# Optimization experiments

Measured on AMD Instinct MI355X. Metric: run time of the kernel, lower is better.

The kernel has to match this reference:

```python
import jax, jax.numpy as jnp
import numpy as np
import math

RATIOS = [2, 4, 8, 16]   # attn_aggr_ratio per path
HEAD_DIM = 64
EPS = 1e-5               # BatchNorm1d eps (eval mode, running stats)


def _bn(x, g, b, m, v):
    # x: (N, C, L); per-channel eval-mode BatchNorm1d
    inv = g / jnp.sqrt(v + EPS)
    return x * inv[None, :, None] + (b - m * inv)[None, :, None]


def _conv1(x, W, b=None):
    # 1x1 Conv1d == channel matmul. x: (N, Cin, L), W: (Cout, Cin)
    y = jnp.einsum('ncl,dc->ndl', x, W)
    if b is not None:
        y = y + b[None, :, None]
    return y


def setup_inputs() -> dict:
    key = jax.random.key(0)
    ks = iter(jax.random.split(key, 16))
    N, C, L = 8, 512, 3072
    P, d = 4, C // 4
    FF = 4 * C
    w = lambda shape: jax.random.normal(next(ks), shape, dtype=jnp.float32) * 0.05
    inp = {'x': jax.random.normal(next(ks), (N, C, L), dtype=jnp.float32)}
    for nm in ('norm1', 'norm2'):
        inp[nm + '_g'] = jnp.ones((C,), jnp.float32)
        inp[nm + '_b'] = jnp.zeros((C,), jnp.float32)
        inp[nm + '_m'] = jnp.zeros((C,), jnp.float32)
        inp[nm + '_v'] = jnp.ones((C,), jnp.float32)
    for nm in ('Wq', 'Wk', 'Wv', 'Wo', 'Wp'):
        inp[nm] = w((P, d, d))
    for nm in ('bq', 'bk', 'bv', 'bo'):
        inp[nm] = jnp.zeros((P, d), jnp.float32)
    for nm in ('ag', 'an'):  # aggr-block BN and pre-KV BN, per path
        inp[nm + '_g'] = jnp.ones((P, d), jnp.float32)
        inp[nm + '_b'] = jnp.zeros((P, d), jnp.float32)
        inp[nm + '_m'] = jnp.zeros((P, d), jnp.float32)
        inp[nm + '_v'] = jnp.ones((P, d), jnp.float32)
    inp['W1'] = w((FF, C)); inp['b1'] = jnp.zeros((FF,), jnp.float32)
    inp['W2'] = w((C, FF)); inp['b2'] = jnp.zeros((C,), jnp.float32)
    return inp


def reference(x, norm1_g, norm1_b, norm1_m, norm1_v,
              Wq, bq, Wk, bk, Wv, bv, Wo, bo, Wp,
              ag_g, ag_b, ag_m, ag_v, an_g, an_b, an_m, an_v,
              norm2_g, norm2_b, norm2_m, norm2_v,
              W1, b1, W2, b2):
    N, C, L = x.shape
    P = len(RATIOS)
    d = C // P
    h = _bn(x, norm1_g, norm1_b, norm1_m, norm1_v)
    outs = []
    for i, r in enumerate(RATIOS):  # small fixed set of paths
        xi = h[:, i * d:(i + 1) * d, :]                       # (N, d, L)
        q = _conv1(xi, Wq[i], bq[i])                          # (N, d, L)
        # local aware aggregation: avg_pool + max_pool (L divisible by r)
        xp = xi.reshape(N, d, L // r, r)
        xa = xp.mean(-1) + xp.max(-1)                         # (N, d, L/r)
        xa = _bn(_conv1(xa, Wp[i]), ag_g[i], ag_b[i], ag_m[i], ag_v[i])
        xa = _bn(xa, an_g[i], an_b[i], an_m[i], an_v[i])
        k = _conv1(xa, Wk[i], bk[i])
        v = _conv1(xa, Wv[i], bv[i])
        Nh = d // HEAD_DIM
        Lk = L // r
        qh = q.reshape(N, Nh, HEAD_DIM, L) / math.sqrt(HEAD_DIM)
        kh = k.reshape(N, Nh, HEAD_DIM, Lk)
        vh = v.reshape(N, Nh, HEAD_DIM, Lk)
        attn = jax.nn.softmax(jnp.einsum('nhel,nhem->nhlm', qh, kh), axis=-1)
        o = jnp.einsum('nhlm,nhem->nhel', attn, vh).reshape(N, d, L)
        outs.append(_conv1(o, Wo[i], bo[i]))
    x = x + jnp.concatenate(outs, axis=1)                     # residual
    h2 = _bn(x, norm2_g, norm2_b, norm2_m, norm2_v)
    m = jax.nn.gelu(_conv1(h2, W1, b1))
    m = _conv1(m, W2, b2)
    return x + m
```

## Files before the change

kernel.cpp:

```cpp
#include <hip/hip_runtime.h>
#include <math.h>

#define EPS 1e-5f

#define F_BIAS  1
#define F_DBN   2
#define F_GELU  4
#define F_RESID 8

typedef __attribute__((ext_vector_type(8))) __bf16 bf16x8;
typedef __attribute__((ext_vector_type(4))) float f32x4;
typedef __attribute__((ext_vector_type(8))) unsigned short u16x8;

__device__ __forceinline__ unsigned int pack2bf(float a, float b) {
    unsigned short ua = __builtin_bit_cast(unsigned short, (__bf16)a);
    unsigned short ub = __builtin_bit_cast(unsigned short, (__bf16)b);
    return (unsigned int)ua | ((unsigned int)ub << 16);
}

__device__ __forceinline__ void gload_lds16(const unsigned short* g, unsigned short* l) {
    __builtin_amdgcn_global_load_lds(
        (const __attribute__((address_space(1))) unsigned int*)g,
        (__attribute__((address_space(3))) unsigned int*)l,
        16, 0, 0);
}

__device__ __forceinline__ float gelu_f(float u) {
    float s = u * u;
    float w = u * fmaf(s, 0.0713548162726f, 1.59576912161f);
    float e = __expf(-w);
    return u * __builtin_amdgcn_rcpf(1.f + e);
}

__device__ __constant__ int c_LKS[4]  = {1536, 768, 384, 192};
__device__ __constant__ int c_OFFB[4] = {0, 1572864, 2359296, 2752512};

__global__ __launch_bounds__(256) void wcvt_kernel(
    const float* __restrict__ Wq, const float* __restrict__ Wk,
    const float* __restrict__ Wv, const float* __restrict__ Wo,
    const float* __restrict__ Wp, const float* __restrict__ W1,
    const float* __restrict__ W2, unsigned short* __restrict__ dst)
{
    const int WSZ = 65536;
    const int FSZ = 1048576;
    int i4 = blockIdx.x * blockDim.x + threadIdx.x;
    long long i = (long long)i4 * 4;
    const long long total = 5LL * WSZ + 2LL * FSZ;
    if (i >= total) return;
    #pragma unroll
    for (int j = 0; j < 4; ++j) {
        long long idx = i + j;
        float v;
        if      (idx < WSZ)            v = Wq[idx];
        else if (idx < 2 * WSZ)        v = Wk[idx - WSZ];
        else if (idx < 3 * WSZ)        v = Wv[idx - 2 * WSZ];
        else if (idx < 4 * WSZ)        v = Wo[idx - 3 * WSZ];
        else if (idx < 5 * WSZ)        v = Wp[idx - 4 * WSZ];
        else if (idx < 5 * WSZ + FSZ)  v = W1[idx - 5 * WSZ];
        else                           v = W2[idx - 5 * WSZ - FSZ];
        dst[idx] = __builtin_bit_cast(unsigned short, (__bf16)v);
    }
}

__global__ __launch_bounds__(256) void bn_transpose_kernel(
    const float* __restrict__ x,
    const float* __restrict__ g, const float* __restrict__ b,
    const float* __restrict__ bm, const float* __restrict__ bvv,
    unsigned short* __restrict__ hT, int C, int L)
{
    __shared__ float ps[64][65];
    const int l0 = blockIdx.x * 64, ct = blockIdx.y, n = blockIdx.z;
    const int tid = threadIdx.x;
    const int c = tid >> 2, q = tid & 3;
    const int cg = ct * 64 + c;
    float inv = g[cg] * rsqrtf(bvv[cg] + EPS);
    float add = b[cg] - bm[cg] * inv;
    const float* xp = x + ((size_t)n * C + cg) * L + l0 + q * 16;
    #pragma unroll
    for (int s = 0; s < 4; ++s) {
        float4 vv = *(const float4*)&xp[s * 4];
        ps[c][q * 16 + s * 4 + 0] = fmaf(vv.x, inv, add);
        ps[c][q * 16 + s * 4 + 1] = fmaf(vv.y, inv, add);
        ps[c][q * 16 + s * 4 + 2] = fmaf(vv.z, inv, add);
        ps[c][q * 16 + s * 4 + 3] = fmaf(vv.w, inv, add);
    }
    __syncthreads();
    #pragma unroll
    for (int j = 0; j < 2; ++j) {
        int row = (tid >> 3) + 32 * j;
        int cc0 = (tid & 7) * 8;
        unsigned int w0 = pack2bf(ps[cc0 + 0][row], ps[cc0 + 1][row]);
        unsigned int w1 = pack2bf(ps[cc0 + 2][row], ps[cc0 + 3][row]);
        unsigned int w2 = pack2bf(ps[cc0 + 4][row], ps[cc0 + 5][row]);
        unsigned int w3 = pack2bf(ps[cc0 + 6][row], ps[cc0 + 7][row]);
        *(uint4*)&hT[((size_t)n * L + l0 + row) * C + ct * 64 + cc0] =
            make_uint4(w0, w1, w2, w3);
    }
}

__global__ __launch_bounds__(256) void pool_bn_all_kernel(
    const float* __restrict__ x,
    const float* __restrict__ g, const float* __restrict__ b,
    const float* __restrict__ bm, const float* __restrict__ bvv,
    unsigned short* __restrict__ xa0T_all, int C, int L)
{
    const int p = blockIdx.z & 3;
    const int n = blockIdx.z >> 2;
    const int Lk = c_LKS[p];
    const int lk0 = blockIdx.x * 64;
    if (lk0 >= Lk) return;
    const int r = L / Lk;
    const int ct = blockIdx.y;
    __shared__ float ps[64][65];
    const int tid = threadIdx.x;
    const int c = tid >> 2, q = tid & 3;
    const int cg = p * 128 + ct * 64 + c;
    float inv = g[cg] * rsqrtf(bvv[cg] + EPS);
    float add = b[cg] - bm[cg] * inv;
    const float* xp = x + ((size_t)n * C + cg) * L;
    float rinv = 1.0f / (float)r;
    #pragma unroll
    for (int s = 0; s < 16; ++s) {
        int lk = q * 16 + s;
        const float* base = xp + (size_t)(lk0 + lk) * r;
        float sum = 0.f, mx = -INFINITY;
        for (int j = 0; j < r; j += 2) {
            float2 vv = *(const float2*)&base[j];
            float t0 = fmaf(vv.x, inv, add);
            float t1 = fmaf(vv.y, inv, add);
            sum += t0 + t1;
            mx = fmaxf(mx, fmaxf(t0, t1));
        }
        ps[c][lk] = sum * rinv + mx;
    }
    __syncthreads();
    unsigned short* dst = xa0T_all + c_OFFB[p];
    #pragma unroll
    for (int j = 0; j < 2; ++j) {
        int row = (tid >> 3) + 32 * j;
        int cc0 = (tid & 7) * 8;
        unsigned int w0 = pack2bf(ps[cc0 + 0][row], ps[cc0 + 1][row]);
        unsigned int w1 = pack2bf(ps[cc0 + 2][row], ps[cc0 + 3][row]);
        unsigned int w2 = pack2bf(ps[cc0 + 4][row], ps[cc0 + 5][row]);
        unsigned int w3 = pack2bf(ps[cc0 + 6][row], ps[cc0 + 7][row]);
        *(uint4*)&dst[((size_t)n * Lk + lk0 + row) * 128 + ct * 64 + cc0] =
            make_uint4(w0, w1, w2, w3);
    }
}

template<int OMODE>
__global__ __launch_bounds__(256) void gemm_bf(
    const unsigned short* __restrict__ A, const unsigned short* __restrict__ BT,
    int M, int K, int Npos, int ldBT, long long strideBT,
    const float* __restrict__ bias, float oscale, int flags,
    const float* __restrict__ g1, const float* __restrict__ b1p,
    const float* __restrict__ m1p, const float* __restrict__ v1p,
    const float* __restrict__ g2, const float* __restrict__ b2p,
    const float* __restrict__ m2p, const float* __restrict__ v2p,
    float* __restrict__ outN, long long strideN,
    const float* __restrict__ resid, long long strideR,
    unsigned short* __restrict__ outT, int ldT, int moff, long long strideT,
    int gKoff)
{
    __shared__ __align__(16) unsigned short As[2][128][32];
    __shared__ __align__(16) unsigned short Bs[2][128][32];

    const int tid = threadIdx.x;

    const int gdx = gridDim.x, gdy = gridDim.y;
    const int nwg = gdx * gdy * gridDim.z;
    int bid = blockIdx.x + gdx * (blockIdx.y + gdy * blockIdx.z);
    {
        int q = nwg >> 3, rr = nwg & 7;
        int xcd = bid & 7, idx = bid >> 3;
        bid = (xcd < rr ? xcd * (q + 1) : rr * (q + 1) + (xcd - rr) * q) + idx;
    }
    const int bx = bid % gdx;
    const int by = (bid / gdx) % gdy;
    const int bz = bid / (gdx * gdy);

    const int m0 = by * 128;
    const int p0 = bx * 128;
    const unsigned short* Bn = BT + (size_t)bz * strideBT
                              + (size_t)(m0 >> 7) * gKoff;

    const int wave = tid >> 6;
    const int lane = tid & 63;
    const int qcol = lane & 15;
    const int hi   = lane >> 4;
    const int wr   = wave >> 1;
    const int wc   = wave & 1;
    const int lrow = lane >> 2;
    const int lseg = (lane & 3) * 8;

    const unsigned short* aR0 = A + (size_t)(m0 + wave * 32 + lrow) * K + lseg;
    const unsigned short* aR1 = aR0 + (size_t)16 * K;
    int pr0 = p0 + wave * 32 + lrow;      if (pr0 > Npos - 1) pr0 = Npos - 1;
    int pr1 = p0 + wave * 32 + 16 + lrow; if (pr1 > Npos - 1) pr1 = Npos - 1;
    const unsigned short* bR0 = Bn + (size_t)pr0 * ldBT + lseg;
    const unsigned short* bR1 = Bn + (size_t)pr1 * ldBT + lseg;
    unsigned short* ldsA0 = &As[0][wave * 32][0];
    unsigned short* ldsA1 = &As[0][wave * 32 + 16][0];
    unsigned short* ldsB0 = &Bs[0][wave * 32][0];
    unsigned short* ldsB1 = &Bs[0][wave * 32 + 16][0];
    const int bufStride = 128 * 32;

    auto STAGE = [&](int b, int t) {
        const int ko = t * 32;
        gload_lds16(aR0 + ko, ldsA0 + b * bufStride);
        gload_lds16(aR1 + ko, ldsA1 + b * bufStride);
        gload_lds16(bR0 + ko, ldsB0 + b * bufStride);
        gload_lds16(bR1 + ko, ldsB1 + b * bufStride);
    };

    f32x4 acc[4][4] = {};
    const int nt = K >> 5;

    STAGE(0, 0);
    STAGE(1, 1);

    auto MFMA_STEP = [&](int b) {
        bf16x8 af[4], bfr[4];
        #pragma unroll
        for (int mi = 0; mi < 4; ++mi)
            af[mi] = *(const bf16x8*)&As[b][wr * 64 + mi * 16 + qcol][hi * 8];
        #pragma unroll
        for (int ni = 0; ni < 4; ++ni)
            bfr[ni] = *(const bf16x8*)&Bs[b][wc * 64 + ni * 16 + qcol][hi * 8];
        #pragma unroll
        for (int mi = 0; mi < 4; ++mi)
            #pragma unroll
            for (int ni = 0; ni < 4; ++ni)
                acc[mi][ni] = __builtin_amdgcn_mfma_f32_16x16x32_bf16(
                    af[mi], bfr[ni], acc[mi][ni], 0, 0, 0);
    };

    int cur = 0;
    for (int t = 0; t < nt - 1; ++t) {
        asm volatile("s_waitcnt vmcnt(4)" ::: "memory");
        __builtin_amdgcn_s_barrier();
        MFMA_STEP(cur);
        __builtin_amdgcn_s_barrier();
        if (t + 2 < nt) STAGE(cur, t + 2);
        cur ^= 1;
    }
    asm volatile("s_waitcnt vmcnt(0)" ::: "memory");
    __builtin_amdgcn_s_barrier();
    MFMA_STEP(cur);

    float* Cn = outN + (size_t)bz * strideN;
    const float* Rn = resid + (size_t)bz * strideR;
    unsigned short* Tn = outT + (size_t)bz * strideT;

    #pragma unroll
    for (int mi = 0; mi < 4; ++mi) {
        const int mb = m0 + wr * 64 + mi * 16 + hi * 4;
        float4 bv4 = make_float4(0.f, 0.f, 0.f, 0.f);
        if (flags & F_BIAS) bv4 = *(const float4*)&bias[mb];
        float s1[4], t1[4];
        if ((flags & F_DBN) || OMODE == 3) {
            float4 gg = *(const float4*)&g1[mb];
            float4 bb = *(const float4*)&b1p[mb];
            float4 mm = *(const float4*)&m1p[mb];
            float4 vv = *(const float4*)&v1p[mb];
            float gga[4] = {gg.x, gg.y, gg.z, gg.w};
            float bba[4] = {bb.x, bb.y, bb.z, bb.w};
            float mma[4] = {mm.x, mm.y, mm.z, mm.w};
            float vva[4] = {vv.x, vv.y, vv.z, vv.w};
            #pragma unroll
            for (int r2 = 0; r2 < 4; ++r2) {
                float iv = gga[r2] * rsqrtf(vva[r2] + EPS);
                s1[r2] = iv; t1[r2] = bba[r2] - mma[r2] * iv;
            }
        }
        float s2[4], t2[4];
        if (flags & F_DBN) {
            float4 gg = *(const float4*)&g2[mb];
            float4 bb = *(const float4*)&b2p[mb];
            float4 mm = *(const float4*)&m2p[mb];
            float4 vv = *(const float4*)&v2p[mb];
            float gga[4] = {gg.x, gg.y, gg.z, gg.w};
            float bba[4] = {bb.x, bb.y, bb.z, bb.w};
            float mma[4] = {mm.x, mm.y, mm.z, mm.w};
            float vva[4] = {vv.x, vv.y, vv.z, vv.w};
            #pragma unroll
            for (int r2 = 0; r2 < 4; ++r2) {
                float iv = gga[r2] * rsqrtf(vva[r2] + EPS);
                s2[r2] = iv; t2[r2] = bba[r2] - mma[r2] * iv;
            }
        }
        const float ba[4] = {bv4.x, bv4.y, bv4.z, bv4.w};
        #pragma unroll
        for (int ni = 0; ni < 4; ++ni) {
            const int cp = p0 + wc * 64 + ni * 16 + qcol;
            if (cp >= Npos) continue;
            float vals[4];
            #pragma unroll
            for (int r2 = 0; r2 < 4; ++r2) {
                float val = (acc[mi][ni][r2] + ba[r2]) * oscale;
                if (flags & F_DBN) {
                    val = fmaf(val, s1[r2], t1[r2]);
                    val = fmaf(val, s2[r2], t2[r2]);
                }
                if (flags & F_GELU) val = gelu_f(val);
                vals[r2] = val;
            }
            if (OMODE == 0 || OMODE == 3) {
                #pragma unroll
                for (int r2 = 0; r2 < 4; ++r2) {
                    size_t off = (size_t)(mb + r2) * Npos + cp;
                    float v = vals[r2];
                    if (flags & F_RESID) v += Rn[off];
                    Cn[off] = v;
                    vals[r2] = v;
                }
            }
            if (OMODE == 1) {
                *(uint2*)&Tn[(size_t)cp * ldT + moff + mb] =
                    make_uint2(pack2bf(vals[0], vals[1]), pack2bf(vals[2], vals[3]));
            }
            if (OMODE == 2) {
                #pragma unroll
                for (int r2 = 0; r2 < 4; ++r2)
                    Tn[(size_t)(mb + r2) * Npos + cp] =
                        __builtin_bit_cast(unsigned short, (__bf16)vals[r2]);
            }
            if (OMODE == 3) {
                float a0 = fmaf(vals[0], s1[0], t1[0]);
                float a1 = fmaf(vals[1], s1[1], t1[1]);
                float a2 = fmaf(vals[2], s1[2], t1[2]);
                float a3 = fmaf(vals[3], s1[3], t1[3]);
                *(uint2*)&Tn[(size_t)cp * ldT + moff + mb] =
                    make_uint2(pack2bf(a0, a1), pack2bf(a2, a3));
            }
        }
    }
}

template<int MODE>
__global__ __launch_bounds__(256) void gemm_path(
    const unsigned short* __restrict__ A0, const unsigned short* __restrict__ A1,
    const unsigned short* __restrict__ Bsrc,
    const float* __restrict__ bias0, const float* __restrict__ bias1,
    const float* __restrict__ agg, const float* __restrict__ agb,
    const float* __restrict__ agm, const float* __restrict__ agv,
    const float* __restrict__ ang, const float* __restrict__ anb,
    const float* __restrict__ anm, const float* __restrict__ anv,
    unsigned short* __restrict__ out0, unsigned short* __restrict__ out1)
{
    __shared__ __align__(16) unsigned short As[2][128][32];
    __shared__ __align__(16) unsigned short Bs[2][128][32];

    const int tid = threadIdx.x;
    const int gdx = gridDim.x, gdy = gridDim.y;
    const int nwg = gdx * gdy * gridDim.z;
    int bid = blockIdx.x + gdx * (blockIdx.y + gdy * blockIdx.z);
    {
        int q = nwg >> 3, rr = nwg & 7;
        int xcd = bid & 7, idx = bid >> 3;
        bid = (xcd < rr ? xcd * (q + 1) : rr * (q + 1) + (xcd - rr) * q) + idx;
    }
    const int bx = bid % gdx;
    const int by = (bid / gdx) % gdy;
    const int bz = bid / (gdx * gdy);

    int p, px;
    if      (bx < 12) { p = 0; px = bx; }
    else if (bx < 18) { p = 1; px = bx - 12; }
    else if (bx < 21) { p = 2; px = bx - 18; }
    else              { p = 3; px = bx - 21; }
    const int Lk = c_LKS[p];
    const int offb = c_OFFB[p];
    const int c0 = p * 128;
    const int p0 = px * 128;
    const int K = 128;

    const unsigned short* A = (MODE == 1 && by == 1 ? A1 : A0) + p * 16384;
    const unsigned short* Bn = Bsrc + offb + (size_t)bz * Lk * 128;

    const int wave = tid >> 6;
    const int lane = tid & 63;
    const int qcol = lane & 15;
    const int hi   = lane >> 4;
    const int wr   = wave >> 1;
    const int wc   = wave & 1;
    const int lrow = lane >> 2;
    const int lseg = (lane & 3) * 8;

    const unsigned short* aR0 = A + (size_t)(wave * 32 + lrow) * K + lseg;
    const unsigned short* aR1 = aR0 + (size_t)16 * K;
    int pr0 = p0 + wave * 32 + lrow;      if (pr0 > Lk - 1) pr0 = Lk - 1;
    int pr1 = p0 + wave * 32 + 16 + lrow; if (pr1 > Lk - 1) pr1 = Lk - 1;
    const unsigned short* bR0 = Bn + (size_t)pr0 * 128 + lseg;
    const unsigned short* bR1 = Bn + (size_t)pr1 * 128 + lseg;
    unsigned short* ldsA0 = &As[0][wave * 32][0];
    unsigned short* ldsA1 = &As[0][wave * 32 + 16][0];
    unsigned short* ldsB0 = &Bs[0][wave * 32][0];
    unsigned short* ldsB1 = &Bs[0][wave * 32 + 16][0];
    const int bufStride = 128 * 32;

    auto STAGE = [&](int b, int t) {
        const int ko = t * 32;
        gload_lds16(aR0 + ko, ldsA0 + b * bufStride);
        gload_lds16(aR1 + ko, ldsA1 + b * bufStride);
        gload_lds16(bR0 + ko, ldsB0 + b * bufStride);
        gload_lds16(bR1 + ko, ldsB1 + b * bufStride);
    };

    f32x4 acc[4][4] = {};
    STAGE(0, 0);
    STAGE(1, 1);

    auto MFMA_STEP = [&](int b) {
        bf16x8 af[4], bfr[4];
        #pragma unroll
        for (int mi = 0; mi < 4; ++mi)
            af[mi] = *(const bf16x8*)&As[b][wr * 64 + mi * 16 + qcol][hi * 8];
        #pragma unroll
        for (int ni = 0; ni < 4; ++ni)
            bfr[ni] = *(const bf16x8*)&Bs[b][wc * 64 + ni * 16 + qcol][hi * 8];
        #pragma unroll
        for (int mi = 0; mi < 4; ++mi)
            #pragma unroll
            for (int ni = 0; ni < 4; ++ni)
                acc[mi][ni] = __builtin_amdgcn_mfma_f32_16x16x32_bf16(
                    af[mi], bfr[ni], acc[mi][ni], 0, 0, 0);
    };

    int cur = 0;
    const int nt = 4;
    for (int t = 0; t < nt - 1; ++t) {
        asm volatile("s_waitcnt vmcnt(4)" ::: "memory");
        __builtin_amdgcn_s_barrier();
        MFMA_STEP(cur);
        __builtin_amdgcn_s_barrier();
        if (t + 2 < nt) STAGE(cur, t + 2);
        cur ^= 1;
    }
    asm volatile("s_waitcnt vmcnt(0)" ::: "memory");
    __builtin_amdgcn_s_barrier();
    MFMA_STEP(cur);

    const bool isV = (MODE == 1 && by == 1);
    unsigned short* Tn = (isV ? out1 : out0) + offb + (size_t)bz * Lk * 128;
    const float* bias = (MODE == 0) ? nullptr : (by == 0 ? bias0 : bias1);

    #pragma unroll
    for (int mi = 0; mi < 4; ++mi) {
        const int mb = wr * 64 + mi * 16 + hi * 4;
        float ba[4] = {0.f, 0.f, 0.f, 0.f};
        if (MODE == 1) {
            float4 bv4 = *(const float4*)&bias[c0 + mb];
            ba[0] = bv4.x; ba[1] = bv4.y; ba[2] = bv4.z; ba[3] = bv4.w;
        }
        float s1[4], t1[4], s2[4], t2[4];
        if (MODE == 0) {
            #pragma unroll
            for (int r2 = 0; r2 < 4; ++r2) {
                int gm = c0 + mb + r2;
                float i1 = agg[gm] * rsqrtf(agv[gm] + EPS);
                s1[r2] = i1; t1[r2] = agb[gm] - agm[gm] * i1;
                float i2 = ang[gm] * rsqrtf(anv[gm] + EPS);
                s2[r2] = i2; t2[r2] = anb[gm] - anm[gm] * i2;
            }
        }
        #pragma unroll
        for (int ni = 0; ni < 4; ++ni) {
            const int cp = p0 + wc * 64 + ni * 16 + qcol;
            if (cp >= Lk) continue;
            float vals[4];
            #pragma unroll
            for (int r2 = 0; r2 < 4; ++r2) {
                float val = acc[mi][ni][r2] + ba[r2];
                if (MODE == 0) {
                    val = fmaf(val, s1[r2], t1[r2]);
                    val = fmaf(val, s2[r2], t2[r2]);
                }
                vals[r2] = val;
            }
            if (!isV) {
                *(uint2*)&Tn[(size_t)cp * 128 + mb] =
                    make_uint2(pack2bf(vals[0], vals[1]), pack2bf(vals[2], vals[3]));
            } else {
                #pragma unroll
                for (int r2 = 0; r2 < 4; ++r2)
                    Tn[(size_t)(mb + r2) * Lk + cp] =
                        __builtin_bit_cast(unsigned short, (__bf16)vals[r2]);
            }
        }
    }
}

__global__ __launch_bounds__(256) void attn_bf_all_kernel(
    const unsigned short* __restrict__ qT, const unsigned short* __restrict__ kT_all,
    const unsigned short* __restrict__ vN_all, unsigned short* __restrict__ obT,
    int L)
{
    const int p = blockIdx.z;
    const int Lk = c_LKS[p];
    const int offb = c_OFFB[p];
    const int l0 = blockIdx.x * 64;
    const int nh = blockIdx.y;
    const int n = nh >> 1, h = nh & 1;
    const unsigned short* qn = qT + (size_t)n * L * 512 + p * 128 + h * 64;
    const unsigned short* kn = kT_all + offb + (size_t)n * Lk * 128 + h * 64;
    const unsigned short* vn = vN_all + offb + ((size_t)n * 128 + h * 64) * Lk;
    unsigned short*       on = obT + (size_t)n * L * 512 + p * 128 + h * 64;

    __shared__ __align__(16) unsigned short Ks[2][64][64];
    __shared__ __align__(16) unsigned short Vs[2][64][64];
    __shared__ __align__(16) unsigned short Ps[4][16][72];

    const int tid = threadIdx.x;
    const int wave = tid >> 6;
    const int lane = tid & 63;
    const int qcol = lane & 15;
    const int hi   = lane >> 4;
    const int ql   = wave * 16 + qcol;

    const int srow = lane >> 3;
    const int sxor = (lane & 7) ^ srow;
    const unsigned short* kS0 = kn + (size_t)(wave * 16 + srow) * 128 + sxor * 8;
    const unsigned short* kS1 = kn + (size_t)(wave * 16 + 8 + srow) * 128 + sxor * 8;
    const unsigned short* vS0 = vn + (size_t)(wave * 16 + srow) * Lk + sxor * 8;
    const unsigned short* vS1 = vn + (size_t)(wave * 16 + 8 + srow) * Lk + sxor * 8;
    unsigned short* ldsK0 = &Ks[0][wave * 16][0];
    unsigned short* ldsK1 = &Ks[0][wave * 16 + 8][0];
    unsigned short* ldsV0 = &Vs[0][wave * 16][0];
    unsigned short* ldsV1 = &Vs[0][wave * 16 + 8][0];
    const int bufStride = 64 * 64;

    auto STAGE = [&](int b, int t) {
        const int mc = t * 64;
        gload_lds16(kS0 + (size_t)mc * 128, ldsK0 + b * bufStride);
        gload_lds16(kS1 + (size_t)mc * 128, ldsK1 + b * bufStride);
        gload_lds16(vS0 + mc, ldsV0 + b * bufStride);
        gload_lds16(vS1 + mc, ldsV1 + b * bufStride);
    };

    const int x0 = (hi ^ (qcol & 7)) * 8;
    const int x1 = x0 ^ 32;

    bf16x8 qf0 = *(const bf16x8*)&qn[(size_t)(l0 + ql) * 512 + hi * 8];
    bf16x8 qf1 = *(const bf16x8*)&qn[(size_t)(l0 + ql) * 512 + 32 + hi * 8];

    f32x4 o_acc[4] = {};
    float mrow = -INFINITY, lrow = 0.f;
    const int nt = Lk >> 6;

    STAGE(0, 0);
    STAGE(1, 1);

    auto COMPUTE = [&](int b) {
        f32x4 sacc[4];
        #pragma unroll
        for (int kt = 0; kt < 4; ++kt) {
            bf16x8 k0 = *(const bf16x8*)&Ks[b][kt * 16 + qcol][x0];
            bf16x8 k1 = *(const bf16x8*)&Ks[b][kt * 16 + qcol][x1];
            f32x4 a = {};
            a = __builtin_amdgcn_mfma_f32_16x16x32_bf16(k0, qf0, a, 0, 0, 0);
            a = __builtin_amdgcn_mfma_f32_16x16x32_bf16(k1, qf1, a, 0, 0, 0);
            sacc[kt] = a;
        }
        float m0 = fmaxf(fmaxf(sacc[0][0], sacc[0][1]), fmaxf(sacc[0][2], sacc[0][3]));
        float m1 = fmaxf(fmaxf(sacc[1][0], sacc[1][1]), fmaxf(sacc[1][2], sacc[1][3]));
        float m2 = fmaxf(fmaxf(sacc[2][0], sacc[2][1]), fmaxf(sacc[2][2], sacc[2][3]));
        float m3 = fmaxf(fmaxf(sacc[3][0], sacc[3][1]), fmaxf(sacc[3][2], sacc[3][3]));
        float cm = fmaxf(fmaxf(m0, m1), fmaxf(m2, m3));
        cm = fmaxf(cm, __shfl_xor(cm, 16));
        cm = fmaxf(cm, __shfl_xor(cm, 32));
        float nm = fmaxf(mrow, cm);
        float alpha = __expf(mrow - nm);
        float csum = 0.f;
        unsigned int pw[4][2];
        #pragma unroll
        for (int kt = 0; kt < 4; ++kt) {
            float p0 = __expf(sacc[kt][0] - nm);
            float p1 = __expf(sacc[kt][1] - nm);
            float p2 = __expf(sacc[kt][2] - nm);
            float p3 = __expf(sacc[kt][3] - nm);
            csum += (p0 + p1) + (p2 + p3);
            pw[kt][0] = pack2bf(p0, p1);
            pw[kt][1] = pack2bf(p2, p3);
        }
        csum += __shfl_xor(csum, 16);
        csum += __shfl_xor(csum, 32);
        lrow = lrow * alpha + csum;
        mrow = nm;

        #pragma unroll
        for (int kt = 0; kt < 4; ++kt)
            *(uint2*)&Ps[wave][qcol][kt * 16 + hi * 4] =
                make_uint2(pw[kt][0], pw[kt][1]);

        #pragma unroll
        for (int et = 0; et < 4; ++et)
            #pragma unroll
            for (int r2 = 0; r2 < 4; ++r2) o_acc[et][r2] *= alpha;

        bf16x8 pf0 = *(const bf16x8*)&Ps[wave][qcol][hi * 8];
        bf16x8 pf1 = *(const bf16x8*)&Ps[wave][qcol][hi * 8 + 32];
        #pragma unroll
        for (int et = 0; et < 4; ++et) {
            bf16x8 v0 = *(const bf16x8*)&Vs[b][et * 16 + qcol][x0];
            bf16x8 v1 = *(const bf16x8*)&Vs[b][et * 16 + qcol][x1];
            o_acc[et] = __builtin_amdgcn_mfma_f32_16x16x32_bf16(v0, pf0, o_acc[et], 0, 0, 0);
            o_acc[et] = __builtin_amdgcn_mfma_f32_16x16x32_bf16(v1, pf1, o_acc[et], 0, 0, 0);
        }
    };

    int cur = 0;
    for (int t = 0; t < nt - 1; ++t) {
        asm volatile("s_waitcnt vmcnt(4)" ::: "memory");
        __builtin_amdgcn_s_barrier();
        COMPUTE(cur);
        __builtin_amdgcn_s_barrier();
        if (t + 2 < nt) STAGE(cur, t + 2);
        cur ^= 1;
    }
    asm volatile("s_waitcnt vmcnt(0)" ::: "memory");
    __builtin_amdgcn_s_barrier();
    COMPUTE(cur);

    float invl = 1.f / lrow;
    #pragma unroll
    for (int et = 0; et < 4; ++et) {
        float a0 = o_acc[et][0] * invl, a1 = o_acc[et][1] * invl;
        float a2 = o_acc[et][2] * invl, a3 = o_acc[et][3] * invl;
        *(uint2*)&on[(size_t)(l0 + ql) * 512 + et * 16 + hi * 4] =
            make_uint2(pack2bf(a0, a1), pack2bf(a2, a3));
    }
}

extern "C" void kernel_launch(void* const* d_in, const int* in_sizes, int n_in,
                              void* d_out, int out_size, void* d_ws, size_t ws_size,
                              hipStream_t stream)
{
    const float* x   = (const float*)d_in[0];
    const float* n1g = (const float*)d_in[1];
    const float* n1b = (const float*)d_in[2];
    const float* n1m = (const float*)d_in[3];
    const float* n1v = (const float*)d_in[4];
    const float* n2g = (const float*)d_in[5];
    const float* n2b = (const float*)d_in[6];
    const float* n2m = (const float*)d_in[7];
    const float* n2v = (const float*)d_in[8];
    const float* Wq  = (const float*)d_in[9];
    const float* Wk  = (const float*)d_in[10];
    const float* Wv  = (const float*)d_in[11];
    const float* Wo  = (const float*)d_in[12];
    const float* Wp  = (const float*)d_in[13];
    const float* bq  = (const float*)d_in[14];
    const float* bk  = (const float*)d_in[15];
    const float* bv  = (const float*)d_in[16];
    const float* bo  = (const float*)d_in[17];
    const float* agg = (const float*)d_in[18];
    const float* agb = (const float*)d_in[19];
    const float* agm = (const float*)d_in[20];
    const float* agv = (const float*)d_in[21];
    const float* ang = (const float*)d_in[22];
    const float* anb = (const float*)d_in[23];
    const float* anm = (const float*)d_in[24];
    const float* anv = (const float*)d_in[25];
    const float* W1  = (const float*)d_in[26];
    const float* b1  = (const float*)d_in[27];
    const float* W2  = (const float*)d_in[28];
    const float* b2  = (const float*)d_in[29];

    float* out = (float*)d_out;
    unsigned short* wsb = (unsigned short*)d_ws;

    const int N = 8, Cc = 512, L = 3072, FF = 2048;
    const int WSZ = 65536, FSZ = 1048576;
    const size_t PATHBUF = 2949120;

    unsigned short* wbf      = wsb;
    unsigned short* hT       = wbf      + 5 * WSZ + 2 * FSZ;
    unsigned short* h2T      = hT;
    unsigned short* obT      = hT       + (size_t)N * L * Cc;
    unsigned short* xa0T_all = obT      + (size_t)N * L * 512;
    unsigned short* xabT_all = xa0T_all + PATHBUF;
    unsigned short* kT_all   = xabT_all + PATHBUF;
    unsigned short* vN_all   = kT_all   + PATHBUF;
    unsigned short* m1T      = vN_all   + PATHBUF;
    unsigned short* qTall    = m1T;

    const unsigned short* WqB = wbf;
    const unsigned short* WkB = wbf + WSZ;
    const unsigned short* WvB = wbf + 2 * WSZ;
    const unsigned short* WoB = wbf + 3 * WSZ;
    const unsigned short* WpB = wbf + 4 * WSZ;
    const unsigned short* W1B = wbf + 5 * WSZ;
    const unsigned short* W2B = wbf + 5 * WSZ + FSZ;

    const float* nul = nullptr;
    float* nulf = nullptr;
    unsigned short* nulu = nullptr;

    {
        long long tot4 = (5LL * WSZ + 2LL * FSZ) / 4;
        wcvt_kernel<<<dim3((unsigned)((tot4 + 255) / 256)), dim3(256), 0, stream>>>(
            Wq, Wk, Wv, Wo, Wp, W1, W2, wbf);
    }
    bn_transpose_kernel<<<dim3(L / 64, Cc / 64, N), dim3(256), 0, stream>>>(
        x, n1g, n1b, n1m, n1v, hT, Cc, L);

    pool_bn_all_kernel<<<dim3(24, 2, N * 4), dim3(256), 0, stream>>>(
        x, n1g, n1b, n1m, n1v, xa0T_all, Cc, L);

    gemm_bf<1><<<dim3(L / 128, 4, N), dim3(256), 0, stream>>>(
        WqB, hT, 512, 128, L, Cc, (long long)L * Cc,
        bq, 0.125f, F_BIAS,
        nul, nul, nul, nul, nul, nul, nul, nul,
        nulf, 0, nul, 0, qTall, 512, 0, (long long)L * 512, 128);

    gemm_path<0><<<dim3(23, 1, N), dim3(256), 0, stream>>>(
        WpB, nulu, xa0T_all, nul, nul,
        agg, agb, agm, agv, ang, anb, anm, anv,
        xabT_all, nulu);

    gemm_path<1><<<dim3(23, 2, N), dim3(256), 0, stream>>>(
        WkB, WvB, xabT_all, bk, bv,
        nul, nul, nul, nul, nul, nul, nul, nul,
        kT_all, vN_all);

    attn_bf_all_kernel<<<dim3(L / 64, N * 2, 4), dim3(256), 0, stream>>>(
        qTall, kT_all, vN_all, obT, L);

    gemm_bf<3><<<dim3(L / 128, 4, N), dim3(256), 0, stream>>>(
        WoB, obT, 512, 128, L, 512, (long long)L * 512,
        bo, 1.f, F_BIAS | F_RESID,
        n2g, n2b, n2m, n2v,
        nul, nul, nul, nul,
        out, (long long)Cc * L,
        x, (long long)Cc * L,
        h2T, Cc, 0, (long long)L * Cc, 128);

    gemm_bf<1><<<dim3(L / 128, FF / 128, N), dim3(256), 0, stream>>>(
        W1B, h2T, FF, Cc, L, Cc, (long long)L * Cc,
        b1, 1.f, F_BIAS | F_GELU,
        nul, nul, nul, nul, nul, nul, nul, nul,
        nulf, 0, nul, 0, m1T, FF, 0, (long long)L * FF, 0);

    gemm_bf<0><<<dim3(L / 128, Cc / 128, N), dim3(256), 0, stream>>>(
        W2B, m1T, Cc, FF, L, FF, (long long)L * FF,
        b2, 1.f, F_BIAS | F_RESID,
        nul, nul, nul, nul, nul, nul, nul, nul,
        out, (long long)Cc * L, out, (long long)Cc * L,
        nulu, 0, 0, 0, 0);
}
```

Baseline: 532.7 us.

## Add 256x256-tile 512-thread bf16 GEMM with XCD remap for MLP layers

```diff
diff --git a/kernel.cpp b/kernel.cpp
--- a/kernel.cpp
+++ b/kernel.cpp
@@ -332,6 +332,142 @@
                 float a3 = fmaf(vals[3], s1[3], t1[3]);
                 *(uint2*)&Tn[(size_t)cp * ldT + moff + mb] =
                     make_uint2(pack2bf(a0, a1), pack2bf(a2, a3));
+            }
+        }
+    }
+}
+
+template<int OMODE, int FLAGS>
+__global__ __launch_bounds__(512, 1) void gemm_bf256(
+    const unsigned short* __restrict__ A, const unsigned short* __restrict__ BT,
+    int K, int Npos, int ldBT, long long strideBT,
+    const float* __restrict__ bias,
+    float* __restrict__ outN, long long strideN,
+    const float* __restrict__ resid, long long strideR,
+    unsigned short* __restrict__ outT, int ldT, long long strideT)
+{
+    __shared__ __align__(16) unsigned short As[2][256][64];
+    __shared__ __align__(16) unsigned short Bs[2][256][64];
+
+    const int tid = threadIdx.x;
+
+    const int gdx = gridDim.x, gdy = gridDim.y;
+    const int nwg = gdx * gdy * gridDim.z;
+    int bid = blockIdx.x + gdx * (blockIdx.y + gdy * blockIdx.z);
+    {
+        int q = nwg >> 3, rr = nwg & 7;
+        int xcd = bid & 7, idx = bid >> 3;
+        bid = (xcd < rr ? xcd * (q + 1) : rr * (q + 1) + (xcd - rr) * q) + idx;
+    }
+    const int bx = bid % gdx;
+    const int by = (bid / gdx) % gdy;
+    const int bz = bid / (gdx * gdy);
+
+    const int m0 = by * 256;
+    const int p0 = bx * 256;
+    const unsigned short* Bn = BT + (size_t)bz * strideBT;
+
+    const int wave = tid >> 6;
+    const int lane = tid & 63;
+    const int qcol = lane & 15;
+    const int hi   = lane >> 4;
+    const int wr   = wave >> 2;
+    const int wc   = wave & 3;
+
+    const int srow = lane >> 3;
+    const int sxor = ((lane & 7) ^ srow) * 8;
+
+    const unsigned short* aS = A + (size_t)(m0 + wave * 32 + srow) * K + sxor;
+    const unsigned short* bS = Bn + (size_t)(p0 + wave * 32 + srow) * ldBT + sxor;
+    unsigned short* ldsA = &As[0][wave * 32][0];
+    unsigned short* ldsB = &Bs[0][wave * 32][0];
+    const int bufStride = 256 * 64;
+
+    auto STAGE = [&](int b, int t) {
+        const int ko = t * 64;
+        #pragma unroll
+        for (int j = 0; j < 4; ++j) {
+            gload_lds16(aS + (size_t)(j * 8) * K + ko,
+                        ldsA + b * bufStride + j * 8 * 64);
+            gload_lds16(bS + (size_t)(j * 8) * ldBT + ko,
+                        ldsB + b * bufStride + j * 8 * 64);
+        }
+    };
+
+    const int xr0 = (hi ^ (qcol & 7)) * 8;
+
+    f32x4 acc[8][4] = {};
+    const int nt = K >> 6;
+
+    STAGE(0, 0);
+    STAGE(1, 1);
+
+    auto MFMA_STEP = [&](int b) {
+        #pragma unroll
+        for (int kk = 0; kk < 2; ++kk) {
+            const int xx = xr0 ^ (kk << 5);
+            bf16x8 af[8], bfr[4];
+            #pragma unroll
+            for (int mi = 0; mi < 8; ++mi)
+                af[mi] = *(const bf16x8*)&As[b][wr * 128 + mi * 16 + qcol][xx];
+            #pragma unroll
+            for (int ni = 0; ni < 4; ++ni)
+                bfr[ni] = *(const bf16x8*)&Bs[b][wc * 64 + ni * 16 + qcol][xx];
+            #pragma unroll
+            for (int mi = 0; mi < 8; ++mi)
+                #pragma unroll
+                for (int ni = 0; ni < 4; ++ni)
+                    acc[mi][ni] = __builtin_amdgcn_mfma_f32_16x16x32_bf16(
+                        af[mi], bfr[ni], acc[mi][ni], 0, 0, 0);
+        }
+    };
+
+    int cur = 0;
+    for (int t = 0; t < nt - 1; ++t) {
+        asm volatile("s_waitcnt vmcnt(8)" ::: "memory");
+        __builtin_amdgcn_s_barrier();
+        MFMA_STEP(cur);
+        __builtin_amdgcn_s_barrier();
+        if (t + 2 < nt) STAGE(cur, t + 2);
+        cur ^= 1;
+    }
+    asm volatile("s_waitcnt vmcnt(0)" ::: "memory");
+    __builtin_amdgcn_s_barrier();
+    MFMA_STEP(cur);
+
+    float* Cn = outN + (size_t)bz * strideN;
+    const float* Rn = resid + (size_t)bz * strideR;
+    unsigned short* Tn = outT + (size_t)bz * strideT;
+
+    #pragma unroll
+    for (int mi = 0; mi < 8; ++mi) {
+        const int mb = m0 + wr * 128 + mi * 16 + hi * 4;
+        float ba[4] = {0.f, 0.f, 0.f, 0.f};
+        if (FLAGS & F_BIAS) {
+            float4 bv4 = *(const float4*)&bias[mb];
+            ba[0] = bv4.x; ba[1] = bv4.y; ba[2] = bv4.z; ba[3] = bv4.w;
+        }
+        #pragma unroll
+        for (int ni = 0; ni < 4; ++ni) {
+            const int cp = p0 + wc * 64 + ni * 16 + qcol;
+            float vals[4];
+            #pragma unroll
+            for (int r2 = 0; r2 < 4; ++r2) {
+                float val = acc[mi][ni][r2] + ba[r2];
+                if (FLAGS & F_GELU) val = gelu_f(val);
+                vals[r2] = val;
+            }
+            if (OMODE == 0) {
+                #pragma unroll
+                for (int r2 = 0; r2 < 4; ++r2) {
+                    size_t off = (size_t)(mb + r2) * Npos + cp;
+                    float v = vals[r2];
+                    if (FLAGS & F_RESID) v += Rn[off];
+                    Cn[off] = v;
+                }
+            } else {
+                *(uint2*)&Tn[(size_t)cp * ldT + mb] =
+                    make_uint2(pack2bf(vals[0], vals[1]), pack2bf(vals[2], vals[3]));
             }
         }
     }
@@ -736,16 +872,15 @@
         x, (long long)Cc * L,
         h2T, Cc, 0, (long long)L * Cc, 128);
 
-    gemm_bf<1><<<dim3(L / 128, FF / 128, N), dim3(256), 0, stream>>>(
-        W1B, h2T, FF, Cc, L, Cc, (long long)L * Cc,
-        b1, 1.f, F_BIAS | F_GELU,
-        nul, nul, nul, nul, nul, nul, nul, nul,
-        nulf, 0, nul, 0, m1T, FF, 0, (long long)L * FF, 0);
-
-    gemm_bf<0><<<dim3(L / 128, Cc / 128, N), dim3(256), 0, stream>>>(
-        W2B, m1T, Cc, FF, L, FF, (long long)L * FF,
-        b2, 1.f, F_BIAS | F_RESID,
-        nul, nul, nul, nul, nul, nul, nul, nul,
+    gemm_bf256<1, F_BIAS | F_GELU><<<dim3(L / 256, FF / 256, N), dim3(512), 0, stream>>>(
+        W1B, h2T, Cc, L, Cc, (long long)L * Cc,
+        b1,
+        nulf, 0, nul, 0,
+        m1T, FF, (long long)L * FF);
+
+    gemm_bf256<0, F_BIAS | F_RESID><<<dim3(L / 256, Cc / 256, N), dim3(512), 0, stream>>>(
+        W2B, m1T, FF, L, FF, (long long)L * FF,
+        b2,
         out, (long long)Cc * L, out, (long long)Cc * L,
-        nulu, 0, 0, 0, 0);
-}
+        nulu, 0, 0);
+}
```

Measured after the change: 517.1 us. 2.9% less time.
